# Kernel optimization log

Measured on AMD Instinct MI355X. Metric: run time of the kernel, lower is better.

The kernel has to match this reference:

```python
import jax, jax.numpy as jnp
import numpy as np
from jax import lax

PAD, EOS, SOS = 0, 1, 2
B, S, V, NT, E, H = 64, 256, 50000, 64, 300, 500  # H = hidden per direction (HIDDEN_SIZE//2)


def setup_inputs():
    key = jax.random.key(0)
    ks = jax.random.split(key, 24)
    x = jax.random.randint(ks[0], (B, S), 1, V)          # no PAD tokens -> mask all ones
    y0 = jax.random.randint(ks[1], (B, S), 3, NT)        # gold tags, avoid special tags
    embed = jax.random.normal(ks[2], (V, E)) * 0.1
    embed = embed.at[PAD].set(0.0)                       # padding_idx=PAD
    inp = {"x": x, "y0": y0, "embed": embed}
    ki = 3
    for l, din in enumerate([E, 2 * H]):                 # layer0 in=E, layer1 in=2H
        for d in ("f", "b"):
            inp[f"w_ih_l{l}{d}"] = jax.random.normal(ks[ki], (4 * H, din)) * 0.05; ki += 1
            inp[f"w_hh_l{l}{d}"] = jax.random.normal(ks[ki], (4 * H, H)) * 0.05; ki += 1
            inp[f"b_l{l}{d}"] = jnp.zeros((4 * H,))       # b_ih + b_hh combined
    inp["W_out"] = jax.random.normal(ks[ki], (NT, 2 * H)) * 0.05; ki += 1
    inp["b_out"] = jnp.zeros((NT,))
    trans = jax.random.normal(ks[ki], (NT, NT))
    trans = trans.at[SOS, :].set(-10000.0).at[:, EOS].set(-10000.0)
    trans = trans.at[:, PAD].set(-10000.0).at[PAD, :].set(-10000.0)
    trans = trans.at[PAD, EOS].set(0.0).at[PAD, PAD].set(0.0)
    inp["trans"] = trans
    return inp


def _lstm_dir(xs, w_ih, w_hh, b, reverse):
    # xs: [B,S,D] -> outputs [B,S,H]; PyTorch gate order i,f,g,o
    def step(carry, x_t):
        h, c = carry
        g = x_t @ w_ih.T + h @ w_hh.T + b
        i, f, gg, o = jnp.split(g, 4, axis=-1)
        c = jax.nn.sigmoid(f) * c + jax.nn.sigmoid(i) * jnp.tanh(gg)
        h = jax.nn.sigmoid(o) * jnp.tanh(c)
        return (h, c), h
    bz = xs.shape[0]
    init = (jnp.zeros((bz, H), xs.dtype), jnp.zeros((bz, H), xs.dtype))
    _, hs = lax.scan(step, init, jnp.swapaxes(xs, 0, 1), reverse=reverse)
    return jnp.swapaxes(hs, 0, 1)


def _forward(x, y0, embed, w_ih_l0f, w_hh_l0f, b_l0f, w_ih_l0b, w_hh_l0b, b_l0b,
             w_ih_l1f, w_hh_l1f, b_l1f, w_ih_l1b, w_hh_l1b, b_l1b, W_out, b_out, trans):
    h0 = embed[x]                                        # [B,S,E]
    h1 = jnp.concatenate([_lstm_dir(h0, w_ih_l0f, w_hh_l0f, b_l0f, False),
                          _lstm_dir(h0, w_ih_l0b, w_hh_l0b, b_l0b, True)], -1)
    h2 = jnp.concatenate([_lstm_dir(h1, w_ih_l1f, w_hh_l1f, b_l1f, False),
                          _lstm_dir(h1, w_ih_l1b, w_hh_l1b, b_l1b, True)], -1)
    mask = (x > 0).astype(h2.dtype)                      # [B,S]
    emit = (h2 @ W_out.T + b_out) * mask[..., None]      # [B,S,NT]
    # --- CRF partition function Z (batched logsumexp DP) ---
    score0 = jnp.full((B, NT), -10000.0, emit.dtype).at[:, SOS].set(0.0)
    def step(score, inp):
        e_t, m_t = inp                                   # [B,NT], [B]
        # new[b,i] = lse_j(score[b,j] + trans[i,j] + e_t[b,i])
        z = score[:, None, :] + trans[None, :, :] + e_t[:, :, None]
        new = jax.nn.logsumexp(z, axis=-1)
        return jnp.where(m_t[:, None] > 0, new, score), None
    scoreZ, _ = lax.scan(step, score0, (jnp.swapaxes(emit, 0, 1), jnp.swapaxes(mask, 0, 1)))
    Z = jax.nn.logsumexp(scoreZ, axis=-1)                # [B]
    # --- gold path score ---
    yext = jnp.concatenate([jnp.full((B, 1), SOS, dtype=y0.dtype), y0], 1)  # [B,S+1]
    e_gold = jnp.take_along_axis(emit, yext[:, 1:, None], axis=-1)[..., 0]   # [B,S]
    t_gold = trans[yext[:, 1:], yext[:, :-1]] * mask                         # [B,S]
    gold = jnp.sum(e_gold + t_gold, axis=1)
    return Z - gold                                      # [B] NLL per sample


def reference(x, y0, embed, w_ih_l0f, w_hh_l0f, b_l0f, w_ih_l0b, w_hh_l0b, b_l0b,
              w_ih_l1f, w_hh_l1f, b_l1f, w_ih_l1b, w_hh_l1b, b_l1b, W_out, b_out, trans):
    return _forward(x, y0, embed, w_ih_l0f, w_hh_l0f, b_l0f, w_ih_l0b, w_hh_l0b, b_l0b,
                    w_ih_l1f, w_hh_l1f, b_l1f, w_ih_l1b, w_hh_l1b, b_l1b, W_out, b_out, trans)
```

## Files before the change

### kernel.cpp

```cpp
#include <hip/hip_runtime.h>
#include <hip/hip_bf16.h>
#include <cstdint>

#define B_ 64
#define S_ 256
#define V_ 50000
#define NT_ 64
#define E_ 300
#define H_ 500
#define SOS_ 2

typedef __hip_bfloat16 bf16;
typedef unsigned short ushort_t;
typedef __attribute__((ext_vector_type(8))) __bf16 v8bf;
typedef __attribute__((ext_vector_type(4))) float f32x4;
typedef __attribute__((ext_vector_type(4))) unsigned int u32x4;

__device__ __forceinline__ float sigm(float x) { return 1.f / (1.f + __expf(-x)); }
__device__ __forceinline__ float tanh_fast(float x) {
    float xx = fminf(fmaxf(x, -15.f), 15.f);
    float e = __expf(2.f * xx);
    return (e - 1.f) / (e + 1.f);
}

__device__ __forceinline__ float bfu_to_f(ushort_t u) {
    unsigned int v = ((unsigned int)u) << 16;
    return __builtin_bit_cast(float, v);
}
__device__ __forceinline__ ushort_t f_to_bfu(float f) {
    return __builtin_bit_cast(ushort_t, __float2bfloat16(f));
}

__device__ __forceinline__ v8bf load16_coh(const ushort_t* p) {
    v8bf r;
    asm volatile("global_load_dwordx4 %0, %1, off sc0 sc1" : "=v"(r) : "v"(p) : "memory");
    return r;
}
__device__ __forceinline__ void store8_coh(ushort_t* p, uint2 v) {
    asm volatile("global_store_dwordx2 %0, %1, off sc0 sc1" :: "v"(p), "v"(v) : "memory");
}

__global__ void dbg_kernel(float* out, float v) {
    if (threadIdx.x < 64) out[threadIdx.x] = v;
}

__global__ void gather_kernel(const int* __restrict__ x, const float* __restrict__ embed,
                              ushort_t* __restrict__ h0) {
    int m = blockIdx.x;
    int tok = x[m];
    const float* src = embed + (size_t)tok * E_;
    ushort_t* dst = h0 + (size_t)m * 320;
    for (int e = threadIdx.x; e < 320; e += blockDim.x)
        dst[e] = (e < E_) ? f_to_bfu(src[e]) : (ushort_t)0;
}

__global__ void conv_w_kernel(const float* __restrict__ in, ushort_t* __restrict__ out,
                              int N, int Kout, int Kin, int split, int real) {
    int idx = blockIdx.x * 256 + threadIdx.x;
    if (idx >= N * Kout) return;
    int n = idx / Kout, k = idx % Kout;
    int half = (k >= split) ? 1 : 0;
    int ki = k - half * split;
    float v = (ki < real) ? in[(size_t)n * Kin + half * real + ki] : 0.f;
    out[idx] = f_to_bfu(v);
}

template <int AV>
__global__ __launch_bounds__(256) void gemm_mfma(const ushort_t* __restrict__ A,
                                                 const ushort_t* __restrict__ Wf,
                                                 const ushort_t* __restrict__ Wb,
                                                 const float* __restrict__ bf_,
                                                 const float* __restrict__ bb_,
                                                 ushort_t* __restrict__ Cf,
                                                 ushort_t* __restrict__ Cb,
                                                 int Nn, int Kp) {
    const ushort_t* W = blockIdx.z ? Wb : Wf;
    const float* bias = blockIdx.z ? bb_ : bf_;
    ushort_t* C = blockIdx.z ? Cb : Cf;
    const int t = blockIdx.x;
    const int n0 = blockIdx.y * 64;
    const int tid = threadIdx.x;
    const int lane = tid & 63;
    const int wv = tid >> 6;
    const int wn = wv & 1, wb = wv >> 1;
    const int l15 = lane & 15, kgrp = lane >> 4;

    __shared__ ushort_t wlds[64 * 64];

    const int rrow = tid >> 3, kc = tid & 7;
    const int rrow2 = (tid + 256) >> 3;

    auto load_tile = [&](int k0, v8bf* nxt) {
#pragma unroll
        for (int c = 0; c < 2; ++c) {
            int rr = c ? rrow2 : rrow;
            int n = n0 + rr, k = k0 + kc * 8;
            if (n < Nn) {
                nxt[c] = *(const v8bf*)(W + (size_t)n * Kp + k);
            } else {
                u32x4 z = {0u, 0u, 0u, 0u};
                nxt[c] = __builtin_bit_cast(v8bf, z);
            }
        }
    };

    f32x4 acc[2][2] = {};
    v8bf nxt[2];
    load_tile(0, nxt);

    for (int k0 = 0; k0 < Kp; k0 += 64) {
        if (k0) __syncthreads();
#pragma unroll
        for (int c = 0; c < 2; ++c) {
            int rr = c ? rrow2 : rrow;
            int off = (rr * 128 + kc * 16) ^ ((rr & 7) << 4);
            *(v8bf*)((char*)wlds + off) = nxt[c];
        }
        __syncthreads();
        if (k0 + 64 < Kp) load_tile(k0 + 64, nxt);

#pragma unroll
        for (int ks = 0; ks < 2; ++ks) {
            int kk = k0 + ks * 32 + kgrp * 8;
            int br0 = wb * 32 + l15;
            const ushort_t* pb0;
            const ushort_t* pb1;
            if (AV == 0) {
                pb0 = A + ((size_t)(br0 * 256 + t)) * 320 + kk;
                pb1 = A + ((size_t)((br0 + 16) * 256 + t)) * 320 + kk;
            } else {
                int dir = kk >> 9, kr = kk & 511;
                pb0 = A + (((size_t)(dir * B_ + br0) * S_) + t) * 512 + kr;
                pb1 = A + (((size_t)(dir * B_ + br0 + 16) * S_) + t) * 512 + kr;
            }
            v8bf b0v = *(const v8bf*)pb0;
            v8bf b1v = *(const v8bf*)pb1;
            int r0 = wn * 32 + l15;
            int aoff0 = (r0 * 128 + ks * 64 + kgrp * 16) ^ ((r0 & 7) << 4);
            int aoff1 = ((r0 + 16) * 128 + ks * 64 + kgrp * 16) ^ ((r0 & 7) << 4);
            v8bf a0 = *(const v8bf*)((const char*)wlds + aoff0);
            v8bf a1 = *(const v8bf*)((const char*)wlds + aoff1);
            acc[0][0] = __builtin_amdgcn_mfma_f32_16x16x32_bf16(a0, b0v, acc[0][0], 0, 0, 0);
            acc[0][1] = __builtin_amdgcn_mfma_f32_16x16x32_bf16(a0, b1v, acc[0][1], 0, 0, 0);
            acc[1][0] = __builtin_amdgcn_mfma_f32_16x16x32_bf16(a1, b0v, acc[1][0], 0, 0, 0);
            acc[1][1] = __builtin_amdgcn_mfma_f32_16x16x32_bf16(a1, b1v, acc[1][1], 0, 0, 0);
        }
    }

#pragma unroll
    for (int nsub = 0; nsub < 2; ++nsub) {
#pragma unroll
        for (int bsub = 0; bsub < 2; ++bsub) {
#pragma unroll
            for (int r = 0; r < 4; ++r) {
                int n = n0 + wn * 32 + nsub * 16 + kgrp * 4 + r;
                if (n < Nn) {
                    int bcol = wb * 32 + bsub * 16 + l15;
                    C[(((size_t)t * 4 + (bcol >> 4)) * Nn + n) * 16 + (bcol & 15)] =
                        f_to_bfu(acc[nsub][bsub][r] + bias[n]);
                }
            }
        }
    }
}

__global__ __launch_bounds__(256) void emit_mfma(const ushort_t* __restrict__ A,
                                                 const ushort_t* __restrict__ W,
                                                 const float* __restrict__ bias,
                                                 float* __restrict__ C) {
    const int t = blockIdx.x;
    const int tid = threadIdx.x;
    const int lane = tid & 63;
    const int wv = tid >> 6;
    const int wn = wv & 1, wb = wv >> 1;
    const int l15 = lane & 15, kgrp = lane >> 4;

    __shared__ ushort_t wlds[64 * 64];

    const int rrow = tid >> 3, kc = tid & 7;
    const int rrow2 = (tid + 256) >> 3;

    auto load_tile = [&](int k0, v8bf* nxt) {
#pragma unroll
        for (int c = 0; c < 2; ++c) {
            int rr = c ? rrow2 : rrow;
            nxt[c] = *(const v8bf*)(W + (size_t)rr * 1024 + k0 + kc * 8);
        }
    };

    f32x4 acc[2][2] = {};
    v8bf nxt[2];
    load_tile(0, nxt);

    for (int k0 = 0; k0 < 1024; k0 += 64) {
        if (k0) __syncthreads();
#pragma unroll
        for (int c = 0; c < 2; ++c) {
            int rr = c ? rrow2 : rrow;
            int off = (rr * 128 + kc * 16) ^ ((rr & 7) << 4);
            *(v8bf*)((char*)wlds + off) = nxt[c];
        }
        __syncthreads();
        if (k0 + 64 < 1024) load_tile(k0 + 64, nxt);

#pragma unroll
        for (int ks = 0; ks < 2; ++ks) {
            int kk = k0 + ks * 32 + kgrp * 8;
            int dir = kk >> 9, kr = kk & 511;
            int br0 = wb * 32 + l15;
            const ushort_t* pb0 = A + (((size_t)(dir * B_ + br0) * S_) + t) * 512 + kr;
            const ushort_t* pb1 = A + (((size_t)(dir * B_ + br0 + 16) * S_) + t) * 512 + kr;
            v8bf b0v = *(const v8bf*)pb0;
            v8bf b1v = *(const v8bf*)pb1;
            int r0 = wn * 32 + l15;
            int aoff0 = (r0 * 128 + ks * 64 + kgrp * 16) ^ ((r0 & 7) << 4);
            int aoff1 = ((r0 + 16) * 128 + ks * 64 + kgrp * 16) ^ ((r0 & 7) << 4);
            v8bf a0 = *(const v8bf*)((const char*)wlds + aoff0);
            v8bf a1 = *(const v8bf*)((const char*)wlds + aoff1);
            acc[0][0] = __builtin_amdgcn_mfma_f32_16x16x32_bf16(a0, b0v, acc[0][0], 0, 0, 0);
            acc[0][1] = __builtin_amdgcn_mfma_f32_16x16x32_bf16(a0, b1v, acc[0][1], 0, 0, 0);
            acc[1][0] = __builtin_amdgcn_mfma_f32_16x16x32_bf16(a1, b0v, acc[1][0], 0, 0, 0);
            acc[1][1] = __builtin_amdgcn_mfma_f32_16x16x32_bf16(a1, b1v, acc[1][1], 0, 0, 0);
        }
    }

#pragma unroll
    for (int nsub = 0; nsub < 2; ++nsub) {
#pragma unroll
        for (int bsub = 0; bsub < 2; ++bsub) {
            int n = wn * 32 + nsub * 16 + kgrp * 4;
            int bcol = wb * 32 + bsub * 16 + l15;
            float4 v;
            v.x = acc[nsub][bsub][0] + bias[n + 0];
            v.y = acc[nsub][bsub][1] + bias[n + 1];
            v.z = acc[nsub][bsub][2] + bias[n + 2];
            v.w = acc[nsub][bsub][3] + bias[n + 3];
            *(float4*)&C[((size_t)bcol * S_ + t) * 64 + n] = v;
        }
    }
}

__global__ __launch_bounds__(128, 1) void lstm_wave_kernel(
        const ushort_t* __restrict__ Gf, const ushort_t* __restrict__ Gb,
        const float* __restrict__ Whh_f, const float* __restrict__ Whh_b,
        ushort_t* __restrict__ hseq,
        int* __restrict__ flags) {
    const int bid = blockIdx.x;
    const int dir = bid >> 7;
    const int shard = (bid >> 2) & 31;
    const int bgrp = bid & 3;
    const int tid = threadIdx.x;
    const int w = tid >> 6;
    const int lane = tid & 63;
    const int l15 = lane & 15, kgrp = lane >> 4;
    const int batch = bgrp * 16 + l15;
    const int n0c = shard * 16;
    const int domain = dir * 4 + bgrp;

    const ushort_t* G = dir ? Gb : Gf;
    const float* Whh = dir ? Whh_b : Whh_f;

    __shared__ float xlds[2][16][64];

    v8bf wreg[4][8];
    {
        int g = l15 & 3;
        int colbase = n0c + (l15 >> 2) * 4;
#pragma unroll
        for (int j = 0; j < 4; ++j) {
            int col = colbase + j;
            bool cok = col < H_;
            const float* wrow = Whh + ((size_t)g * H_ + (cok ? col : 0)) * H_;
#pragma unroll
            for (int ki = 0; ki < 8; ++ki) {
                union { ushort_t u[8]; v8bf v; } tmp;
#pragma unroll
                for (int e = 0; e < 8; ++e) {
                    int k = w * 256 + ki * 32 + kgrp * 8 + e;
                    tmp.u[e] = (cok && k < H_) ? f_to_bfu(wrow[k]) : (ushort_t)0;
                }
                wreg[j][ki] = tmp.v;
            }
        }
    }

    float c[4] = {0.f, 0.f, 0.f, 0.f};

    for (int s = 0; s < S_; ++s) {
        const int tr = dir ? (S_ - 1 - s) : s;

        float p[4][4];
        if (w == 0) {
#pragma unroll
            for (int j = 0; j < 4; ++j) {
                int col = n0c + kgrp * 4 + j;
                int colc = (col < H_) ? col : (H_ - 1);
#pragma unroll
                for (int g = 0; g < 4; ++g)
                    p[j][g] = bfu_to_f(G[(((size_t)tr * 4 + bgrp) * 2000 + g * H_ + colc) * 16 + l15]);
            }
        }
        asm volatile("" ::: "memory");

        f32x4 acc[4] = {};
        if (s > 0) {
            {
                const int need = s;
                int fi = domain * 32 + w * 16 + (lane & 15);
                while (true) {
                    int f = (lane < 16)
                        ? __hip_atomic_load(&flags[fi], __ATOMIC_RELAXED, __HIP_MEMORY_SCOPE_AGENT)
                        : need;
                    if (__all(f >= need)) break;
                    __builtin_amdgcn_s_sleep(1);
                }
            }
            asm volatile("" ::: "memory");

            const int trp = dir ? (tr + 1) : (tr - 1);
            const ushort_t* hrow = hseq + (((size_t)dir * B_ + batch) * S_ + trp) * 512 + w * 256;
            v8bf bfr[8];
#pragma unroll
            for (int ki = 0; ki < 8; ++ki)
                bfr[ki] = load16_coh(hrow + ki * 32 + kgrp * 8);
            asm volatile("s_waitcnt vmcnt(0)" ::: "memory");
            __builtin_amdgcn_sched_barrier(0);

#pragma unroll
            for (int ki = 0; ki < 8; ++ki)
#pragma unroll
                for (int j = 0; j < 4; ++j)
                    acc[j] = __builtin_amdgcn_mfma_f32_16x16x32_bf16(wreg[j][ki], bfr[ki], acc[j], 0, 0, 0);
        }

        if (w == 1) {
#pragma unroll
            for (int j = 0; j < 4; ++j)
#pragma unroll
                for (int r = 0; r < 4; ++r)
                    xlds[s & 1][j * 4 + r][lane] = acc[j][r];
        }
        __syncthreads();

        if (w == 0) {
            ushort_t hv[4];
#pragma unroll
            for (int j = 0; j < 4; ++j) {
                float gi = p[j][0] + acc[j][0] + xlds[s & 1][j * 4 + 0][lane];
                float gf = p[j][1] + acc[j][1] + xlds[s & 1][j * 4 + 1][lane];
                float gg = p[j][2] + acc[j][2] + xlds[s & 1][j * 4 + 2][lane];
                float go = p[j][3] + acc[j][3] + xlds[s & 1][j * 4 + 3][lane];
                c[j] = sigm(gf) * c[j] + sigm(gi) * tanh_fast(gg);
                hv[j] = f_to_bfu(sigm(go) * tanh_fast(c[j]));
            }
            int colb = n0c + kgrp * 4;
            if (colb < H_) {
                uint2 pk;
                pk.x = (unsigned)hv[0] | ((unsigned)hv[1] << 16);
                pk.y = (unsigned)hv[2] | ((unsigned)hv[3] << 16);
                store8_coh(hseq + (((size_t)dir * B_ + batch) * S_ + tr) * 512 + colb, pk);
            }
            asm volatile("s_waitcnt vmcnt(0)" ::: "memory");
            if (lane == 0)
                __hip_atomic_store(&flags[domain * 32 + shard], s + 1,
                                   __ATOMIC_RELAXED, __HIP_MEMORY_SCOPE_AGENT);
        }
    }
}

__global__ __launch_bounds__(256) void crf_kernel(const float* __restrict__ emit,
                                                  const float* __restrict__ trans,
                                                  const int* __restrict__ x,
                                                  const int* __restrict__ y0,
                                                  float* __restrict__ out) {
    const int b = blockIdx.x, tid = threadIdx.x;
    __shared__ float tr[64][65];
    __shared__ float sc[2][64];
    __shared__ float zsh;
    __shared__ float red[4];

    for (int e = tid; e < 4096; e += 256) tr[e >> 6][e & 63] = trans[e];
    if (tid < 64) sc[0][tid] = (tid == SOS_) ? 0.f : -10000.f;
    __syncthreads();

    const int i = tid >> 2, sub = tid & 3;
    int cur = 0;
    for (int t = 0; t < S_; ++t) {
        int m = x[b * S_ + t] > 0;
        float v[16];
        float vmax = -3.0e38f;
#pragma unroll
        for (int jj = 0; jj < 16; ++jj) {
            int j = (sub << 4) + jj;
            v[jj] = sc[cur][j] + tr[i][j];
            vmax = fmaxf(vmax, v[jj]);
        }
        vmax = fmaxf(vmax, __shfl_xor(vmax, 1, 64));
        vmax = fmaxf(vmax, __shfl_xor(vmax, 2, 64));
        float s = 0.f;
#pragma unroll
        for (int jj = 0; jj < 16; ++jj) s += __expf(v[jj] - vmax);
        s += __shfl_xor(s, 1, 64);
        s += __shfl_xor(s, 2, 64);
        float lse = vmax + __logf(s);
        float e_i = emit[((size_t)b * S_ + t) * NT_ + i];
        if (sub == 0) sc[cur ^ 1][i] = m ? (lse + e_i) : sc[cur][i];
        __syncthreads();
        cur ^= 1;
    }

    if (tid < 64) {
        float v2 = sc[cur][tid];
        float mz = v2;
        for (int d = 1; d < 64; d <<= 1) mz = fmaxf(mz, __shfl_xor(mz, d, 64));
        float sz = __expf(v2 - mz);
        for (int d = 1; d < 64; d <<= 1) sz += __shfl_xor(sz, d, 64);
        if (tid == 0) zsh = mz + __logf(sz);
    }
    __syncthreads();

    {
        int t = tid;
        int m = x[b * S_ + t] > 0;
        int yc = y0[b * S_ + t];
        int yp = t ? y0[b * S_ + t - 1] : SOS_;
        float term = m ? (emit[((size_t)b * S_ + t) * NT_ + yc] + tr[yc][yp]) : 0.f;
        for (int d = 1; d < 64; d <<= 1) term += __shfl_xor(term, d, 64);
        if ((tid & 63) == 0) red[tid >> 6] = term;
    }
    __syncthreads();
    if (tid == 0) out[b] = zsh - (red[0] + red[1] + red[2] + red[3]);
}

extern "C" void kernel_launch(void* const* d_in, const int* in_sizes, int n_in,
                              void* d_out, int out_size, void* d_ws, size_t ws_size,
                              hipStream_t stream) {
    const int* x = (const int*)d_in[0];
    const int* y0 = (const int*)d_in[1];
    const float* embed = (const float*)d_in[2];
    const float* w_ih_l0f = (const float*)d_in[3];
    const float* w_hh_l0f = (const float*)d_in[4];
    const float* b_l0f = (const float*)d_in[5];
    const float* w_ih_l0b = (const float*)d_in[6];
    const float* w_hh_l0b = (const float*)d_in[7];
    const float* b_l0b = (const float*)d_in[8];
    const float* w_ih_l1f = (const float*)d_in[9];
    const float* w_hh_l1f = (const float*)d_in[10];
    const float* b_l1f = (const float*)d_in[11];
    const float* w_ih_l1b = (const float*)d_in[12];
    const float* w_hh_l1b = (const float*)d_in[13];
    const float* b_l1b = (const float*)d_in[14];
    const float* W_out = (const float*)d_in[15];
    const float* b_out = (const float*)d_in[16];
    const float* trans = (const float*)d_in[17];
    float* outp = (float*)d_out;

    char* ws = (char*)d_ws;
    size_t off = 0;
    auto alloc = [&](size_t bytes) {
        void* p = ws + off;
        off += (bytes + 255) & ~(size_t)255;
        return p;
    };
    ushort_t* h0 = (ushort_t*)alloc((size_t)B_ * S_ * 320 * 2);
    ushort_t* hseq = (ushort_t*)alloc((size_t)2 * B_ * S_ * 512 * 2);
    float* emitb = (float*)alloc((size_t)B_ * S_ * NT_ * 4);
    ushort_t* Gf = (ushort_t*)alloc((size_t)S_ * 2000 * 64 * 2);
    ushort_t* Gb = (ushort_t*)alloc((size_t)S_ * 2000 * 64 * 2);
    int* flags = (int*)alloc((size_t)2 * 256 * 4);
    (void)in_sizes; (void)n_in; (void)out_size;

    ushort_t* Wl0f = (ushort_t*)emitb;
    ushort_t* Wl0b = Wl0f + (size_t)2000 * 320;
    ushort_t* Wl1f = (ushort_t*)h0;
    ushort_t* Wl1b = Wl1f + (size_t)2000 * 1024;
    ushort_t* Wout = Wl1b + (size_t)2000 * 1024;

    if (off > ws_size) {
        dbg_kernel<<<1, 64, 0, stream>>>(outp, (float)(ws_size / 1048576.0));
        return;
    }

    const int M = B_ * S_;

    hipMemsetAsync(flags, 0, (size_t)2 * 256 * 4, stream);
    hipMemsetAsync(hseq, 0, (size_t)2 * B_ * S_ * 512 * 2, stream);

    gather_kernel<<<M, 128, 0, stream>>>(x, embed, h0);

    {
        int tot = 2000 * 320, nb = (tot + 255) / 256;
        conv_w_kernel<<<nb, 256, 0, stream>>>(w_ih_l0f, Wl0f, 2000, 320, 300, 320, 300);
        conv_w_kernel<<<nb, 256, 0, stream>>>(w_ih_l0b, Wl0b, 2000, 320, 300, 320, 300);
    }

    gemm_mfma<0><<<dim3(S_, 32, 2), 256, 0, stream>>>(
        h0, Wl0f, Wl0b, b_l0f, b_l0b, Gf, Gb, 2000, 320);

    {
        int tot = 2000 * 1024, nb = (tot + 255) / 256;
        conv_w_kernel<<<nb, 256, 0, stream>>>(w_ih_l1f, Wl1f, 2000, 1024, 1000, 512, 500);
        conv_w_kernel<<<nb, 256, 0, stream>>>(w_ih_l1b, Wl1b, 2000, 1024, 1000, 512, 500);
        int tot2 = 64 * 1024, nb2 = (tot2 + 255) / 256;
        conv_w_kernel<<<nb2, 256, 0, stream>>>(W_out, Wout, 64, 1024, 1000, 512, 500);
    }

    lstm_wave_kernel<<<256, 128, 0, stream>>>(Gf, Gb, w_hh_l0f, w_hh_l0b, hseq, flags);

    gemm_mfma<1><<<dim3(S_, 32, 2), 256, 0, stream>>>(
        hseq, Wl1f, Wl1b, b_l1f, b_l1b, Gf, Gb, 2000, 1024);

    lstm_wave_kernel<<<256, 128, 0, stream>>>(Gf, Gb, w_hh_l1f, w_hh_l1b, hseq, flags + 256);

    emit_mfma<<<S_, 256, 0, stream>>>(hseq, Wout, b_out, emitb);

    crf_kernel<<<B_, 256, 0, stream>>>(emitb, trans, x, y0, outp);
}
```

Baseline: 2.738 ms.

## Repartition LSTM recurrence into fewer wider blocks with four-way K split

```diff
diff --git a/kernel.cpp b/kernel.cpp
--- a/kernel.cpp
+++ b/kernel.cpp
@@ -36,8 +36,8 @@
     asm volatile("global_load_dwordx4 %0, %1, off sc0 sc1" : "=v"(r) : "v"(p) : "memory");
     return r;
 }
-__device__ __forceinline__ void store8_coh(ushort_t* p, uint2 v) {
-    asm volatile("global_store_dwordx2 %0, %1, off sc0 sc1" :: "v"(p), "v"(v) : "memory");
+__device__ __forceinline__ void store16_coh(ushort_t* p, u32x4 v) {
+    asm volatile("global_store_dwordx4 %0, %1, off sc0 sc1" :: "v"(p), "v"(v) : "memory");
 }
 
 __global__ void dbg_kernel(float* out, float v) {
@@ -240,75 +240,74 @@
     }
 }
 
-__global__ __launch_bounds__(128, 1) void lstm_wave_kernel(
+__global__ __launch_bounds__(256, 1) void lstm_wave_kernel(
         const ushort_t* __restrict__ Gf, const ushort_t* __restrict__ Gb,
         const float* __restrict__ Whh_f, const float* __restrict__ Whh_b,
         ushort_t* __restrict__ hseq,
         int* __restrict__ flags) {
     const int bid = blockIdx.x;
-    const int dir = bid >> 7;
-    const int shard = (bid >> 2) & 31;
+    const int dir = bid >> 6;
+    const int shard = (bid >> 2) & 15;
     const int bgrp = bid & 3;
     const int tid = threadIdx.x;
     const int w = tid >> 6;
     const int lane = tid & 63;
     const int l15 = lane & 15, kgrp = lane >> 4;
     const int batch = bgrp * 16 + l15;
-    const int n0c = shard * 16;
+    const int n0c = shard * 32;
     const int domain = dir * 4 + bgrp;
 
     const ushort_t* G = dir ? Gb : Gf;
     const float* Whh = dir ? Whh_b : Whh_f;
 
-    __shared__ float xlds[2][16][64];
-
-    v8bf wreg[4][8];
+    __shared__ float xlds[2][3][8][4][64];
+
+    v8bf wreg[8][4];
     {
         int g = l15 & 3;
-        int colbase = n0c + (l15 >> 2) * 4;
-#pragma unroll
-        for (int j = 0; j < 4; ++j) {
-            int col = colbase + j;
+#pragma unroll
+        for (int rt = 0; rt < 8; ++rt) {
+            int col = n0c + (l15 >> 2) * 8 + rt;
             bool cok = col < H_;
             const float* wrow = Whh + ((size_t)g * H_ + (cok ? col : 0)) * H_;
 #pragma unroll
-            for (int ki = 0; ki < 8; ++ki) {
+            for (int ki = 0; ki < 4; ++ki) {
                 union { ushort_t u[8]; v8bf v; } tmp;
 #pragma unroll
                 for (int e = 0; e < 8; ++e) {
-                    int k = w * 256 + ki * 32 + kgrp * 8 + e;
+                    int k = w * 128 + ki * 32 + kgrp * 8 + e;
                     tmp.u[e] = (cok && k < H_) ? f_to_bfu(wrow[k]) : (ushort_t)0;
                 }
-                wreg[j][ki] = tmp.v;
-            }
-        }
-    }
-
-    float c[4] = {0.f, 0.f, 0.f, 0.f};
+                wreg[rt][ki] = tmp.v;
+            }
+        }
+    }
+
+    float c[8] = {};
 
     for (int s = 0; s < S_; ++s) {
         const int tr = dir ? (S_ - 1 - s) : s;
 
-        float p[4][4];
+        float p[8][4];
         if (w == 0) {
 #pragma unroll
-            for (int j = 0; j < 4; ++j) {
-                int col = n0c + kgrp * 4 + j;
+            for (int rt = 0; rt < 8; ++rt) {
+                int col = n0c + kgrp * 8 + rt;
                 int colc = (col < H_) ? col : (H_ - 1);
 #pragma unroll
                 for (int g = 0; g < 4; ++g)
-                    p[j][g] = bfu_to_f(G[(((size_t)tr * 4 + bgrp) * 2000 + g * H_ + colc) * 16 + l15]);
+                    p[rt][g] = bfu_to_f(G[(((size_t)tr * 4 + bgrp) * 2000 + g * H_ + colc) * 16 + l15]);
             }
         }
         asm volatile("" ::: "memory");
 
-        f32x4 acc[4] = {};
+        f32x4 acc[8] = {};
         if (s > 0) {
             {
                 const int need = s;
-                int fi = domain * 32 + w * 16 + (lane & 15);
+                int fi = domain * 16 + w * 4 + (lane & 3);
                 while (true) {
-                    int f = (lane < 16)
+                    int f = (lane < 4)
                         ? __hip_atomic_load(&flags[fi], __ATOMIC_RELAXED, __HIP_MEMORY_SCOPE_AGENT)
                         : need;
                     if (__all(f >= need)) break;
@@ -318,51 +317,61 @@
             asm volatile("" ::: "memory");
 
             const int trp = dir ? (tr + 1) : (tr - 1);
-            const ushort_t* hrow = hseq + (((size_t)dir * B_ + batch) * S_ + trp) * 512 + w * 256;
-            v8bf bfr[8];
-#pragma unroll
-            for (int ki = 0; ki < 8; ++ki)
+            const ushort_t* hrow = hseq + (((size_t)dir * B_ + batch) * S_ + trp) * 512 + w * 128;
+            v8bf bfr[4];
+#pragma unroll
+            for (int ki = 0; ki < 4; ++ki)
                 bfr[ki] = load16_coh(hrow + ki * 32 + kgrp * 8);
             asm volatile("s_waitcnt vmcnt(0)" ::: "memory");
             __builtin_amdgcn_sched_barrier(0);
 
 #pragma unroll
-            for (int ki = 0; ki < 8; ++ki)
-#pragma unroll
-                for (int j = 0; j < 4; ++j)
-                    acc[j] = __builtin_amdgcn_mfma_f32_16x16x32_bf16(wreg[j][ki], bfr[ki], acc[j], 0, 0, 0);
-        }
-
-        if (w == 1) {
-#pragma unroll
-            for (int j = 0; j < 4; ++j)
+            for (int ki = 0; ki < 4; ++ki)
+#pragma unroll
+                for (int rt = 0; rt < 8; ++rt)
+                    acc[rt] = __builtin_amdgcn_mfma_f32_16x16x32_bf16(wreg[rt][ki], bfr[ki], acc[rt], 0, 0, 0);
+        }
+
+        if (w > 0) {
+#pragma unroll
+            for (int rt = 0; rt < 8; ++rt)
 #pragma unroll
                 for (int r = 0; r < 4; ++r)
-                    xlds[s & 1][j * 4 + r][lane] = acc[j][r];
+                    xlds[s & 1][w - 1][rt][r][lane] = acc[rt][r];
         }
         __syncthreads();
 
         if (w == 0) {
-            ushort_t hv[4];
-#pragma unroll
-            for (int j = 0; j < 4; ++j) {
-                float gi = p[j][0] + acc[j][0] + xlds[s & 1][j * 4 + 0][lane];
-                float gf = p[j][1] + acc[j][1] + xlds[s & 1][j * 4 + 1][lane];
-                float gg = p[j][2] + acc[j][2] + xlds[s & 1][j * 4 + 2][lane];
-                float go = p[j][3] + acc[j][3] + xlds[s & 1][j * 4 + 3][lane];
-                c[j] = sigm(gf) * c[j] + sigm(gi) * tanh_fast(gg);
-                hv[j] = f_to_bfu(sigm(go) * tanh_fast(c[j]));
-            }
-            int colb = n0c + kgrp * 4;
-            if (colb < H_) {
-                uint2 pk;
-                pk.x = (unsigned)hv[0] | ((unsigned)hv[1] << 16);
-                pk.y = (unsigned)hv[2] | ((unsigned)hv[3] << 16);
-                store8_coh(hseq + (((size_t)dir * B_ + batch) * S_ + tr) * 512 + colb, pk);
-            }
+            ushort_t hv[8];
+#pragma unroll
+            for (int rt = 0; rt < 8; ++rt) {
+                float gi = p[rt][0] + acc[rt][0];
+                float gf = p[rt][1] + acc[rt][1];
+                float gg = p[rt][2] + acc[rt][2];
+                float go = p[rt][3] + acc[rt][3];
+                if (s > 0) {
+#pragma unroll
+                    for (int q = 0; q < 3; ++q) {
+                        gi += xlds[s & 1][q][rt][0][lane];
+                        gf += xlds[s & 1][q][rt][1][lane];
+                        gg += xlds[s & 1][q][rt][2][lane];
+                        go += xlds[s & 1][q][rt][3][lane];
+                    }
+                }
+                c[rt] = sigm(gf) * c[rt] + sigm(gi) * tanh_fast(gg);
+                float h = sigm(go) * tanh_fast(c[rt]);
+                int col = n0c + kgrp * 8 + rt;
+                hv[rt] = (col < H_) ? f_to_bfu(h) : (ushort_t)0;
+            }
+            u32x4 pk;
+            pk[0] = (unsigned)hv[0] | ((unsigned)hv[1] << 16);
+            pk[1] = (unsigned)hv[2] | ((unsigned)hv[3] << 16);
+            pk[2] = (unsigned)hv[4] | ((unsigned)hv[5] << 16);
+            pk[3] = (unsigned)hv[6] | ((unsigned)hv[7] << 16);
+            store16_coh(hseq + (((size_t)dir * B_ + batch) * S_ + tr) * 512 + n0c + kgrp * 8, pk);
             asm volatile("s_waitcnt vmcnt(0)" ::: "memory");
             if (lane == 0)
-                __hip_atomic_store(&flags[domain * 32 + shard], s + 1,
+                __hip_atomic_store(&flags[domain * 16 + shard], s + 1,
                                    __ATOMIC_RELAXED, __HIP_MEMORY_SCOPE_AGENT);
         }
     }
@@ -505,12 +514,12 @@
         conv_w_kernel<<<nb2, 256, 0, stream>>>(W_out, Wout, 64, 1024, 1000, 512, 500);
     }
 
-    lstm_wave_kernel<<<256, 128, 0, stream>>>(Gf, Gb, w_hh_l0f, w_hh_l0b, hseq, flags);
+    lstm_wave_kernel<<<128, 256, 0, stream>>>(Gf, Gb, w_hh_l0f, w_hh_l0b, hseq, flags);
 
     gemm_mfma<1><<<dim3(S_, 32, 2), 256, 0, stream>>>(
         hseq, Wl1f, Wl1b, b_l1f, b_l1b, Gf, Gb, 2000, 1024);
 
-    lstm_wave_kernel<<<256, 128, 0, stream>>>(Gf, Gb, w_hh_l1f, w_hh_l1b, hseq, flags + 256);
+    lstm_wave_kernel<<<128, 256, 0, stream>>>(Gf, Gb, w_hh_l1f, w_hh_l1b, hseq, flags + 256);
 
     emit_mfma<<<S_, 256, 0, stream>>>(hseq, Wout, b_out, emitb);
 
```

Result: slower. 3.281 ms (+19.8%).
